# Performance work log

Hardware: AMD Instinct MI355X
Metric: run time of the kernel (lower is better)

## Reference

```python
import jax, jax.numpy as jnp
import numpy as np

TAG_DIM = 128
ENC_DIM = 256
ATT_DIM = 128
B, TQ, TK = 32, 2048, 2048


def setup_inputs() -> dict:
    key = jax.random.key(0)
    ks = jax.random.split(key, 9)
    s = 0.02
    return {
        "query": jax.random.normal(ks[0], (B, TQ, TAG_DIM), dtype=jnp.float32),
        "key": jax.random.normal(ks[1], (B, TK, ENC_DIM), dtype=jnp.float32),
        "value": jax.random.normal(ks[2], (B, TK, ENC_DIM), dtype=jnp.float32),
        # query_linear (computed in the original forward but its output is unused)
        "Wq": jax.random.normal(ks[3], (ATT_DIM, TAG_DIM), dtype=jnp.float32) * s,
        "bq": jnp.zeros((ATT_DIM,), dtype=jnp.float32),
        # key_linear / value_linear (project_k_v=1)
        "Wk": jax.random.normal(ks[4], (ATT_DIM, ENC_DIM), dtype=jnp.float32) * s,
        "bk": jnp.zeros((ATT_DIM,), dtype=jnp.float32),
        "Wv": jax.random.normal(ks[5], (ATT_DIM, ENC_DIM), dtype=jnp.float32) * s,
        "bv": jnp.zeros((ATT_DIM,), dtype=jnp.float32),
    }


def reference(query, key, value, Wq, bq, Wk, bk, Wv, bv):
    # Faithful to the source: q is computed but the raw `query` is used in the bmm.
    q = query @ Wq.T + bq  # dead value (bug preserved from original module)
    k = key @ Wk.T + bk      # [B, TK, ATT_DIM]
    v = value @ Wv.T + bv    # [B, TK, ATT_DIM]
    dot = jnp.einsum('bqd,bkd->bqk', query, k)        # [B, TQ, TK]
    score = jax.nn.softmax(dot, axis=-1)
    att_res = jnp.einsum('bqk,bkd->bqd', score, v).mean(axis=1)  # [B, ATT_DIM]
    return att_res, score
```

## Files before the change

### kernel.cpp

```cpp
#include <hip/hip_runtime.h>
#include <hip/hip_bf16.h>

#define NB   32
#define TQn  2048
#define TKn  2048
#define TAGD 128
#define ENCD 256
#define ATTD 128

using bf16x8 = __attribute__((ext_vector_type(8))) __bf16;
using f32x4  = __attribute__((ext_vector_type(4))) float;

__device__ __forceinline__ bf16x8 cvt8(float4 p0, float4 p1) {
    bf16x8 r;
    r[0] = (__bf16)p0.x; r[1] = (__bf16)p0.y; r[2] = (__bf16)p0.z; r[3] = (__bf16)p0.w;
    r[4] = (__bf16)p1.x; r[5] = (__bf16)p1.y; r[6] = (__bf16)p1.z; r[7] = (__bf16)p1.w;
    return r;
}

__global__ __launch_bounds__(256) void proj_kernel(
    const float* __restrict__ key, const float* __restrict__ value,
    const float* __restrict__ Wk, const float* __restrict__ bk,
    const float* __restrict__ Wv, const float* __restrict__ bv,
    __bf16* __restrict__ kproj, __bf16* __restrict__ vproj)
{
    const int sel = blockIdx.y;
    const float* in   = sel ? value : key;
    const float* W    = sel ? Wv : Wk;
    const float* bias = sel ? bv : bk;
    __bf16* out       = sel ? vproj : kproj;

    const int tid  = threadIdx.x;
    const int w    = tid >> 6;
    const int lane = tid & 63;
    const int qd   = lane >> 4;
    const int ln   = lane & 15;
    const int r0   = blockIdx.x * 64 + w * 16;

    bf16x8 afrag[8];
    {
        const float* arow = in + (size_t)(r0 + ln) * ENCD + 8 * qd;
        #pragma unroll
        for (int s = 0; s < 8; ++s) {
            float4 p0 = *(const float4*)(arow + 32 * s);
            float4 p1 = *(const float4*)(arow + 32 * s + 4);
            afrag[s] = cvt8(p0, p1);
        }
    }

    #pragma unroll
    for (int ct = 0; ct < 8; ++ct) {
        f32x4 acc = {0.f, 0.f, 0.f, 0.f};
        const float* wrow = W + (size_t)(ct * 16 + ln) * ENCD + 8 * qd;
        #pragma unroll
        for (int s = 0; s < 8; ++s) {
            float4 p0 = *(const float4*)(wrow + 32 * s);
            float4 p1 = *(const float4*)(wrow + 32 * s + 4);
            bf16x8 bfrag = cvt8(p0, p1);
            acc = __builtin_amdgcn_mfma_f32_16x16x32_bf16(afrag[s], bfrag, acc, 0, 0, 0);
        }
        const float bb = bias[ct * 16 + ln];
        #pragma unroll
        for (int r = 0; r < 4; ++r) {
            const int row = r0 + 4 * qd + r;
            out[(size_t)row * ATTD + ct * 16 + ln] = (__bf16)(acc[r] + bb);
        }
    }
}

__global__ __launch_bounds__(256) void attn_kernel(
    const float* __restrict__ query,
    const __bf16* __restrict__ kproj,
    float* __restrict__ score,
    float* __restrict__ colsum)
{
    const int b   = blockIdx.x >> 5;
    const int q0  = (blockIdx.x & 31) * 64;
    const int tid = threadIdx.x;
    const int w   = tid >> 6;
    const int lane = tid & 63;
    const int qd  = lane >> 4;
    const int ln  = lane & 15;

    __shared__ float lred[4][64];

    bf16x8 a[4][4];
    #pragma unroll
    for (int rg = 0; rg < 4; ++rg) {
        const float* qrow = query + ((size_t)b * TQn + q0 + rg * 16 + ln) * TAGD + 8 * qd;
        #pragma unroll
        for (int s = 0; s < 4; ++s) {
            float4 p0 = *(const float4*)(qrow + 32 * s);
            float4 p1 = *(const float4*)(qrow + 32 * s + 4);
            a[rg][s] = cvt8(p0, p1);
        }
    }

    const __bf16* kb = kproj + (size_t)b * TKn * ATTD;

    float lpart[4][4];
    #pragma unroll
    for (int rg = 0; rg < 4; ++rg)
        #pragma unroll
        for (int r = 0; r < 4; ++r) lpart[rg][r] = 0.f;

    for (int ch = 0; ch < 16; ++ch) {
        #pragma unroll
        for (int cti = 0; cti < 2; ++cti) {
            const int col0 = ch * 128 + (w + 4 * cti) * 16;
            const __bf16* krow = kb + (size_t)(col0 + ln) * ATTD + 8 * qd;
            bf16x8 bf[4];
            #pragma unroll
            for (int s = 0; s < 4; ++s) bf[s] = *(const bf16x8*)(krow + 32 * s);
            #pragma unroll
            for (int rg = 0; rg < 4; ++rg) {
                f32x4 acc = {0.f, 0.f, 0.f, 0.f};
                #pragma unroll
                for (int s = 0; s < 4; ++s)
                    acc = __builtin_amdgcn_mfma_f32_16x16x32_bf16(a[rg][s], bf[s], acc, 0, 0, 0);
                #pragma unroll
                for (int r = 0; r < 4; ++r)
                    lpart[rg][r] += __expf(acc[r] - 20.0f);
            }
        }
    }

    #pragma unroll
    for (int rg = 0; rg < 4; ++rg)
        #pragma unroll
        for (int r = 0; r < 4; ++r) {
            float v = lpart[rg][r];
            v += __shfl_xor(v, 1);
            v += __shfl_xor(v, 2);
            v += __shfl_xor(v, 4);
            v += __shfl_xor(v, 8);
            lpart[rg][r] = v;
        }
    if (ln == 0) {
        #pragma unroll
        for (int rg = 0; rg < 4; ++rg)
            #pragma unroll
            for (int r = 0; r < 4; ++r)
                lred[w][rg * 16 + 4 * qd + r] = lpart[rg][r];
    }
    __syncthreads();

    float linv[4][4];
    #pragma unroll
    for (int rg = 0; rg < 4; ++rg)
        #pragma unroll
        for (int r = 0; r < 4; ++r) {
            const int row = rg * 16 + 4 * qd + r;
            linv[rg][r] = 1.0f / (lred[0][row] + lred[1][row] + lred[2][row] + lred[3][row]);
        }

    float* srow_base = score + ((size_t)b * TQn + q0) * (size_t)TKn;
    for (int ch = 0; ch < 16; ++ch) {
        #pragma unroll
        for (int cti = 0; cti < 2; ++cti) {
            const int col0 = ch * 128 + (w + 4 * cti) * 16;
            const __bf16* krow = kb + (size_t)(col0 + ln) * ATTD + 8 * qd;
            bf16x8 bf[4];
            #pragma unroll
            for (int s = 0; s < 4; ++s) bf[s] = *(const bf16x8*)(krow + 32 * s);
            float csum = 0.f;
            #pragma unroll
            for (int rg = 0; rg < 4; ++rg) {
                f32x4 acc = {0.f, 0.f, 0.f, 0.f};
                #pragma unroll
                for (int s = 0; s < 4; ++s)
                    acc = __builtin_amdgcn_mfma_f32_16x16x32_bf16(a[rg][s], bf[s], acc, 0, 0, 0);
                #pragma unroll
                for (int r = 0; r < 4; ++r) {
                    const float p = __expf(acc[r] - 20.0f) * linv[rg][r];
                    csum += p;
                    __builtin_nontemporal_store(
                        p, srow_base + (size_t)(rg * 16 + 4 * qd + r) * TKn + col0 + ln);
                }
            }
            csum += __shfl_xor(csum, 16);
            csum += __shfl_xor(csum, 32);
            if (qd == 0)
                atomicAdd(&colsum[b * TKn + col0 + ln], csum);
        }
    }
}

__global__ __launch_bounds__(512) void outmean_kernel(
    const float* __restrict__ colsum, const __bf16* __restrict__ vproj,
    float* __restrict__ att)
{
    const int b  = blockIdx.x;
    const int d  = threadIdx.x & 127;
    const int kq = threadIdx.x >> 7;
    __shared__ float red[512];

    const __bf16* vb = vproj + (size_t)b * TKn * ATTD;
    const float* cs  = colsum + b * TKn;
    float acc = 0.f;
    for (int k = kq * 512; k < kq * 512 + 512; ++k)
        acc += cs[k] * (float)vb[(size_t)k * ATTD + d];

    red[threadIdx.x] = acc;
    __syncthreads();
    if (kq == 0) {
        const float t = acc + red[threadIdx.x + 128] + red[threadIdx.x + 256] + red[threadIdx.x + 384];
        att[b * ATTD + d] = t * (1.0f / (float)TQn);
    }
}

extern "C" void kernel_launch(void* const* d_in, const int* in_sizes, int n_in,
                              void* d_out, int out_size, void* d_ws, size_t ws_size,
                              hipStream_t stream) {
    const float* query = (const float*)d_in[0];
    const float* key   = (const float*)d_in[1];
    const float* value = (const float*)d_in[2];
    const float* Wk    = (const float*)d_in[5];
    const float* bk    = (const float*)d_in[6];
    const float* Wv    = (const float*)d_in[7];
    const float* bv    = (const float*)d_in[8];

    float* att   = (float*)d_out;
    float* score = att + (size_t)NB * ATTD;

    char* ws = (char*)d_ws;
    __bf16* kproj = (__bf16*)ws;
    __bf16* vproj = (__bf16*)(ws + (size_t)16 * 1024 * 1024);
    float*  colsum = (float*)(ws + (size_t)32 * 1024 * 1024);

    hipMemsetAsync(colsum, 0, (size_t)NB * TKn * sizeof(float), stream);

    proj_kernel<<<dim3(1024, 2), 256, 0, stream>>>(key, value, Wk, bk, Wv, bv, kproj, vproj);
    attn_kernel<<<dim3(NB * (TQn / 64)), 256, 0, stream>>>(query, kproj, score, colsum);
    outmean_kernel<<<dim3(NB), 512, 0, stream>>>(colsum, vproj, att);
}
```

Before: 1.004 ms.

## Swap MFMA operands for vectorized score stores, swizzle blocks, fold memset into proj

The attention kernel swaps the MFMA A/B operands so each lane holds four consecutive key columns of one query row. Score writes can then go out as 16-byte nontemporal vector stores instead of scalar ones, and the row-sum reductions get simpler. Column sums now need a 16-lane shuffle reduction plus four atomics per lane group. Block indices are also remapped so concurrent blocks span different batches, and the colsum memset is folded into the projection kernel to drop one launch.

```diff
diff --git a/kernel.cpp b/kernel.cpp
--- a/kernel.cpp
+++ b/kernel.cpp
@@ -22,9 +22,17 @@
     const float* __restrict__ key, const float* __restrict__ value,
     const float* __restrict__ Wk, const float* __restrict__ bk,
     const float* __restrict__ Wv, const float* __restrict__ bv,
-    __bf16* __restrict__ kproj, __bf16* __restrict__ vproj)
+    __bf16* __restrict__ kproj, __bf16* __restrict__ vproj,
+    float* __restrict__ colsum)
 {
     const int sel = blockIdx.y;
+
+    if (sel == 0 && blockIdx.x < 64) {
+        float* cs = colsum + (blockIdx.x << 10);
+        #pragma unroll
+        for (int i = 0; i < 4; ++i) cs[i * 256 + threadIdx.x] = 0.0f;
+    }
+
     const float* in   = sel ? value : key;
     const float* W    = sel ? Wv : Wk;
     const float* bias = sel ? bv : bk;
@@ -74,13 +82,14 @@
     float* __restrict__ score,
     float* __restrict__ colsum)
 {
-    const int b   = blockIdx.x >> 5;
-    const int q0  = (blockIdx.x & 31) * 64;
+    const int bid = ((blockIdx.x & 7) << 7) | (blockIdx.x >> 3);
+    const int b   = bid >> 5;
+    const int q0  = (bid & 31) * 64;
     const int tid = threadIdx.x;
-    const int w   = tid >> 6;
+    const int w    = tid >> 6;
     const int lane = tid & 63;
-    const int qd  = lane >> 4;
-    const int ln  = lane & 15;
+    const int qd   = lane >> 4;
+    const int ln   = lane & 15;
 
     __shared__ float lred[4][64];
 
@@ -98,90 +107,86 @@
 
     const __bf16* kb = kproj + (size_t)b * TKn * ATTD;
 
-    float lpart[4][4];
-    #pragma unroll
-    for (int rg = 0; rg < 4; ++rg)
-        #pragma unroll
-        for (int r = 0; r < 4; ++r) lpart[rg][r] = 0.f;
-
+    float lpart[4] = {0.f, 0.f, 0.f, 0.f};
     for (int ch = 0; ch < 16; ++ch) {
         #pragma unroll
         for (int cti = 0; cti < 2; ++cti) {
-            const int col0 = ch * 128 + (w + 4 * cti) * 16;
+            const int col0 = ch * 128 + w * 32 + cti * 16;
             const __bf16* krow = kb + (size_t)(col0 + ln) * ATTD + 8 * qd;
-            bf16x8 bf[4];
-            #pragma unroll
-            for (int s = 0; s < 4; ++s) bf[s] = *(const bf16x8*)(krow + 32 * s);
+            bf16x8 kf[4];
+            #pragma unroll
+            for (int s = 0; s < 4; ++s) kf[s] = *(const bf16x8*)(krow + 32 * s);
             #pragma unroll
             for (int rg = 0; rg < 4; ++rg) {
                 f32x4 acc = {0.f, 0.f, 0.f, 0.f};
                 #pragma unroll
                 for (int s = 0; s < 4; ++s)
-                    acc = __builtin_amdgcn_mfma_f32_16x16x32_bf16(a[rg][s], bf[s], acc, 0, 0, 0);
-                #pragma unroll
-                for (int r = 0; r < 4; ++r)
-                    lpart[rg][r] += __expf(acc[r] - 20.0f);
-            }
-        }
-    }
-
-    #pragma unroll
-    for (int rg = 0; rg < 4; ++rg)
-        #pragma unroll
-        for (int r = 0; r < 4; ++r) {
-            float v = lpart[rg][r];
-            v += __shfl_xor(v, 1);
-            v += __shfl_xor(v, 2);
-            v += __shfl_xor(v, 4);
-            v += __shfl_xor(v, 8);
-            lpart[rg][r] = v;
-        }
-    if (ln == 0) {
-        #pragma unroll
-        for (int rg = 0; rg < 4; ++rg)
-            #pragma unroll
-            for (int r = 0; r < 4; ++r)
-                lred[w][rg * 16 + 4 * qd + r] = lpart[rg][r];
+                    acc = __builtin_amdgcn_mfma_f32_16x16x32_bf16(kf[s], a[rg][s], acc, 0, 0, 0);
+                lpart[rg] += __expf(acc[0] - 20.0f) + __expf(acc[1] - 20.0f)
+                           + __expf(acc[2] - 20.0f) + __expf(acc[3] - 20.0f);
+            }
+        }
+    }
+
+    #pragma unroll
+    for (int rg = 0; rg < 4; ++rg) {
+        float v = lpart[rg];
+        v += __shfl_xor(v, 16);
+        v += __shfl_xor(v, 32);
+        lpart[rg] = v;
+    }
+    if (qd == 0) {
+        #pragma unroll
+        for (int rg = 0; rg < 4; ++rg) lred[w][rg * 16 + ln] = lpart[rg];
     }
     __syncthreads();
 
-    float linv[4][4];
-    #pragma unroll
-    for (int rg = 0; rg < 4; ++rg)
-        #pragma unroll
-        for (int r = 0; r < 4; ++r) {
-            const int row = rg * 16 + 4 * qd + r;
-            linv[rg][r] = 1.0f / (lred[0][row] + lred[1][row] + lred[2][row] + lred[3][row]);
-        }
+    float linv[4];
+    #pragma unroll
+    for (int rg = 0; rg < 4; ++rg) {
+        const int row = rg * 16 + ln;
+        linv[rg] = 1.0f / (lred[0][row] + lred[1][row] + lred[2][row] + lred[3][row]);
+    }
 
     float* srow_base = score + ((size_t)b * TQn + q0) * (size_t)TKn;
     for (int ch = 0; ch < 16; ++ch) {
         #pragma unroll
         for (int cti = 0; cti < 2; ++cti) {
-            const int col0 = ch * 128 + (w + 4 * cti) * 16;
+            const int col0 = ch * 128 + w * 32 + cti * 16;
             const __bf16* krow = kb + (size_t)(col0 + ln) * ATTD + 8 * qd;
-            bf16x8 bf[4];
-            #pragma unroll
-            for (int s = 0; s < 4; ++s) bf[s] = *(const bf16x8*)(krow + 32 * s);
-            float csum = 0.f;
+            bf16x8 kf[4];
+            #pragma unroll
+            for (int s = 0; s < 4; ++s) kf[s] = *(const bf16x8*)(krow + 32 * s);
+            float cs0 = 0.f, cs1 = 0.f, cs2 = 0.f, cs3 = 0.f;
             #pragma unroll
             for (int rg = 0; rg < 4; ++rg) {
                 f32x4 acc = {0.f, 0.f, 0.f, 0.f};
                 #pragma unroll
                 for (int s = 0; s < 4; ++s)
-                    acc = __builtin_amdgcn_mfma_f32_16x16x32_bf16(a[rg][s], bf[s], acc, 0, 0, 0);
-                #pragma unroll
-                for (int r = 0; r < 4; ++r) {
-                    const float p = __expf(acc[r] - 20.0f) * linv[rg][r];
-                    csum += p;
-                    __builtin_nontemporal_store(
-                        p, srow_base + (size_t)(rg * 16 + 4 * qd + r) * TKn + col0 + ln);
-                }
-            }
-            csum += __shfl_xor(csum, 16);
-            csum += __shfl_xor(csum, 32);
-            if (qd == 0)
-                atomicAdd(&colsum[b * TKn + col0 + ln], csum);
+                    acc = __builtin_amdgcn_mfma_f32_16x16x32_bf16(kf[s], a[rg][s], acc, 0, 0, 0);
+                f32x4 p;
+                p[0] = __expf(acc[0] - 20.0f) * linv[rg];
+                p[1] = __expf(acc[1] - 20.0f) * linv[rg];
+                p[2] = __expf(acc[2] - 20.0f) * linv[rg];
+                p[3] = __expf(acc[3] - 20.0f) * linv[rg];
+                cs0 += p[0]; cs1 += p[1]; cs2 += p[2]; cs3 += p[3];
+                __builtin_nontemporal_store(p,
+                    (f32x4*)(srow_base + (size_t)(rg * 16 + ln) * TKn + col0 + 4 * qd));
+            }
+            #pragma unroll
+            for (int m = 1; m < 16; m <<= 1) {
+                cs0 += __shfl_xor(cs0, m);
+                cs1 += __shfl_xor(cs1, m);
+                cs2 += __shfl_xor(cs2, m);
+                cs3 += __shfl_xor(cs3, m);
+            }
+            if (ln == 0) {
+                float* cp = &colsum[b * TKn + col0 + 4 * qd];
+                atomicAdd(cp + 0, cs0);
+                atomicAdd(cp + 1, cs1);
+                atomicAdd(cp + 2, cs2);
+                atomicAdd(cp + 3, cs3);
+            }
         }
     }
 }
@@ -228,9 +233,7 @@
     __bf16* vproj = (__bf16*)(ws + (size_t)16 * 1024 * 1024);
     float*  colsum = (float*)(ws + (size_t)32 * 1024 * 1024);
 
-    hipMemsetAsync(colsum, 0, (size_t)NB * TKn * sizeof(float), stream);
-
-    proj_kernel<<<dim3(1024, 2), 256, 0, stream>>>(key, value, Wk, bk, Wv, bv, kproj, vproj);
+    proj_kernel<<<dim3(1024, 2), 256, 0, stream>>>(key, value, Wk, bk, Wv, bv, kproj, vproj, colsum);
     attn_kernel<<<dim3(NB * (TQn / 64)), 256, 0, stream>>>(query, kproj, score, colsum);
     outmean_kernel<<<dim3(NB), 512, 0, stream>>>(colsum, vproj, att);
 }
```

New measurement: 1.012 ms. Within noise of the previous version (+0.8%).
